# Performance work log

Measured on AMD Instinct MI355X. Metric: run time of the kernel, lower is better.

The kernel has to match this reference:

```python
import jax, jax.numpy as jnp
import numpy as np


def setup_inputs() -> dict:
    key = jax.random.key(0)
    k1, k2 = jax.random.split(key)
    B, H, S, D = 2, 16, 2048, 64
    v = jax.random.normal(k1, (B, H, S, D), dtype=jnp.float32)
    attn_logits = jax.random.normal(k2, (B, H, S, S), dtype=jnp.float32)
    return {"v": v, "attn_logits": attn_logits}


def reference(v, attn_logits):
    # softmax over last axis (keys j), then weighted sum of values
    attn = jax.nn.softmax(attn_logits, axis=-1)  # [b,h,i,j]
    return jnp.einsum('bhij,bhjd->bhid', attn, v)  # [b,h,i,d]
```

## Files before the change

### kernel.cpp

```cpp
#include <hip/hip_runtime.h>
#include <hip/hip_bf16.h>

typedef __attribute__((ext_vector_type(4))) float f32x4;
typedef __attribute__((ext_vector_type(8))) short short8;

#define S_DIM 2048
#define D_DIM 64
#define KB 128
#define NHEADS 32
#define QTILES (S_DIM / 64)
#define NJT (S_DIM / KB)
#define TILE_BYTES (D_DIM * KB * 2)

static __device__ __forceinline__ unsigned short f2bf(float x) {
    union { __hip_bfloat16 h; unsigned short u; } c;
    c.h = __float2bfloat16(x);
    return c.u;
}

__global__ __launch_bounds__(256)
void prep_v(const float* __restrict__ V, unsigned char* __restrict__ blob)
{
    const int b = blockIdx.x, head = b >> 4, jt = b & 15;
    const int t = threadIdx.x, d = t & 63, jg = t >> 6;
    const float* src = V + ((size_t)head * S_DIM + (size_t)jt * KB + jg * 32) * D_DIM + d;
    unsigned char* dst = blob + (size_t)(head * NJT + jt) * TILE_BYTES;
    #pragma unroll
    for (int h = 0; h < 4; ++h) {
        short8 w;
        #pragma unroll
        for (int e = 0; e < 8; ++e)
            w[e] = (short)f2bf(src[(size_t)(h * 8 + e) * D_DIM]);
        const int off = d * 256 + ((jg * 64 + h * 16) ^ ((d & 7) << 4));
        *(short8*)(dst + off) = w;
    }
}

__global__ __launch_bounds__(256, 4)
void attn_main(const float* __restrict__ L,
               const unsigned char* __restrict__ blob,
               float* __restrict__ O)
{
    __shared__ __align__(16) unsigned char vt[2][TILE_BYTES];

    const int tid  = threadIdx.x;
    const int wave = tid >> 6;
    const int lane = tid & 63;
    const int lr   = lane & 15;
    const int lg   = lane >> 4;

    const int bid  = blockIdx.x;
    const int xcd  = bid & 7;
    const int ixd  = bid >> 3;
    const int head = xcd * (NHEADS / 8) + (ixd >> 5);
    const int qt   = ixd & (QTILES - 1);

    const int i0 = qt * 64 + wave * 16;
    const float* lrow = L + ((size_t)head * S_DIM + (size_t)(i0 + lr)) * S_DIM;
    const unsigned char* hblob = blob + (size_t)head * NJT * TILE_BYTES;

    f32x4 acc[4] = {};
    float lsum = 0.0f;
    float pv[32];

    #pragma unroll
    for (int q = 0; q < 4; ++q)
        __builtin_amdgcn_global_load_lds(
            (const __attribute__((address_space(1))) void*)(hblob + q * 4096 + tid * 16),
            (__attribute__((address_space(3))) void*)(&vt[0][q * 4096 + tid * 16]),
            16, 0, 0);
    #pragma unroll
    for (int c = 0; c < 4; ++c) {
        f32x4 a = *(const f32x4*)(lrow + c * 32 + lg * 8);
        f32x4 b = *(const f32x4*)(lrow + c * 32 + lg * 8 + 4);
        pv[c*8+0]=a[0]; pv[c*8+1]=a[1]; pv[c*8+2]=a[2]; pv[c*8+3]=a[3];
        pv[c*8+4]=b[0]; pv[c*8+5]=b[1]; pv[c*8+6]=b[2]; pv[c*8+7]=b[3];
    }
    __syncthreads();

    for (int t = 0; t < NJT; ++t) {
        const int cur = t & 1;

        if (t + 1 < NJT) {
            const unsigned char* nsrc = hblob + (size_t)(t + 1) * TILE_BYTES;
            #pragma unroll
            for (int q = 0; q < 4; ++q)
                __builtin_amdgcn_global_load_lds(
                    (const __attribute__((address_space(1))) void*)(nsrc + q * 4096 + tid * 16),
                    (__attribute__((address_space(3))) void*)(&vt[cur ^ 1][q * 4096 + tid * 16]),
                    16, 0, 0);
        }

        short8 afr[4];
        #pragma unroll
        for (int c = 0; c < 4; ++c) {
            #pragma unroll
            for (int e = 0; e < 8; ++e) {
                float ev = __expf(pv[c*8+e]);
                lsum += ev;
                afr[c][e] = (short)f2bf(ev);
            }
        }

        if (t + 1 < NJT) {
            const float* s = lrow + (size_t)(t + 1) * KB;
            #pragma unroll
            for (int c = 0; c < 4; ++c) {
                f32x4 a = *(const f32x4*)(s + c * 32 + lg * 8);
                f32x4 b = *(const f32x4*)(s + c * 32 + lg * 8 + 4);
                pv[c*8+0]=a[0]; pv[c*8+1]=a[1]; pv[c*8+2]=a[2]; pv[c*8+3]=a[3];
                pv[c*8+4]=b[0]; pv[c*8+5]=b[1]; pv[c*8+6]=b[2]; pv[c*8+7]=b[3];
            }
        }

        #pragma unroll
        for (int c = 0; c < 4; ++c) {
            #pragma unroll
            for (int n = 0; n < 4; ++n) {
                const int off = ((n * 16 + lr) << 8)
                              + (((c << 6) | (lg << 4)) ^ ((lr & 7) << 4));
                short8 bfr = *(const short8*)&vt[cur][off];
                acc[n] = __builtin_amdgcn_mfma_f32_16x16x32_bf16(afr[c], bfr, acc[n], 0, 0, 0);
            }
        }

        __syncthreads();
    }

    lsum += __shfl_xor(lsum, 16);
    lsum += __shfl_xor(lsum, 32);
    #pragma unroll
    for (int r = 0; r < 4; ++r) {
        const float li  = __shfl(lsum, lg * 4 + r);
        const float inv = 1.0f / li;
        float* orow = O + ((size_t)head * S_DIM + (size_t)(i0 + lg * 4 + r)) * D_DIM;
        #pragma unroll
        for (int n = 0; n < 4; ++n)
            orow[n * 16 + lr] = acc[n][r] * inv;
    }
}

extern "C" void kernel_launch(void* const* d_in, const int* in_sizes, int n_in,
                              void* d_out, int out_size, void* d_ws, size_t ws_size,
                              hipStream_t stream) {
    const float* v = (const float*)d_in[0];
    const float* l = (const float*)d_in[1];
    float* out     = (float*)d_out;
    unsigned char* blob = (unsigned char*)d_ws;

    prep_v<<<dim3(NHEADS * NJT), dim3(256), 0, stream>>>(v, blob);
    attn_main<<<dim3(NHEADS * QTILES), dim3(256), 0, stream>>>(l, blob, out);
}
```

Baseline: 124.3 us.

## Coalesce logit loads via per-wave LDS transpose and read V fragments from global

Logits are now loaded as fully coalesced row segments (each half-wave reads 512 contiguous bytes of one row) into a ping-pong register buffer. The exponentiated bf16 values are written to a per-wave swizzled LDS scratch and read back in MFMA A-fragment layout. The shared V tile staging and block-wide barriers are removed, and V B-fragments are read straight from global (likely L2-resident) in a plain transposed layout. The row sum is now accumulated from the rounded bf16 values. The trade is less efficient V fetching from global and extra LDS round-trips, in exchange for better logit coalescing and no __syncthreads.

```diff
diff --git a/kernel.cpp b/kernel.cpp
--- a/kernel.cpp
+++ b/kernel.cpp
@@ -3,136 +3,126 @@
 
 typedef __attribute__((ext_vector_type(4))) float f32x4;
 typedef __attribute__((ext_vector_type(8))) short short8;
+typedef __attribute__((ext_vector_type(2))) unsigned int uint2v;
 
 #define S_DIM 2048
 #define D_DIM 64
 #define KB 128
 #define NHEADS 32
-#define QTILES (S_DIM / 64)
-#define NJT (S_DIM / KB)
-#define TILE_BYTES (D_DIM * KB * 2)
+#define QTILES 32
+#define NJT 16
+#define TILE_USHORT (D_DIM * KB)
 
 static __device__ __forceinline__ unsigned short f2bf(float x) {
     union { __hip_bfloat16 h; unsigned short u; } c;
     c.h = __float2bfloat16(x);
     return c.u;
 }
+static __device__ __forceinline__ float bf2f(unsigned short u) {
+    union { unsigned int i; float f; } c;
+    c.i = ((unsigned int)u) << 16;
+    return c.f;
+}
 
 __global__ __launch_bounds__(256)
-void prep_v(const float* __restrict__ V, unsigned char* __restrict__ blob)
+void prep_v(const float* __restrict__ V, unsigned short* __restrict__ blob)
 {
     const int b = blockIdx.x, head = b >> 4, jt = b & 15;
     const int t = threadIdx.x, d = t & 63, jg = t >> 6;
     const float* src = V + ((size_t)head * S_DIM + (size_t)jt * KB + jg * 32) * D_DIM + d;
-    unsigned char* dst = blob + (size_t)(head * NJT + jt) * TILE_BYTES;
+    unsigned short* dst = blob + (size_t)(head * NJT + jt) * TILE_USHORT + d * KB + jg * 32;
     #pragma unroll
     for (int h = 0; h < 4; ++h) {
         short8 w;
         #pragma unroll
         for (int e = 0; e < 8; ++e)
             w[e] = (short)f2bf(src[(size_t)(h * 8 + e) * D_DIM]);
-        const int off = d * 256 + ((jg * 64 + h * 16) ^ ((d & 7) << 4));
-        *(short8*)(dst + off) = w;
+        *(short8*)(dst + h * 8) = w;
     }
 }
 
-__global__ __launch_bounds__(256, 4)
+__global__ __launch_bounds__(256, 3)
 void attn_main(const float* __restrict__ L,
-               const unsigned char* __restrict__ blob,
+               const unsigned short* __restrict__ blob,
                float* __restrict__ O)
 {
-    __shared__ __align__(16) unsigned char vt[2][TILE_BYTES];
+    __shared__ __align__(16) unsigned char plds[4][4096];
 
     const int tid  = threadIdx.x;
     const int wave = tid >> 6;
     const int lane = tid & 63;
     const int lr   = lane & 15;
     const int lg   = lane >> 4;
+    const int half = lane >> 5;
+    const int l5   = lane & 31;
 
     const int bid  = blockIdx.x;
     const int xcd  = bid & 7;
     const int ixd  = bid >> 3;
     const int head = xcd * (NHEADS / 8) + (ixd >> 5);
     const int qt   = ixd & (QTILES - 1);
+    const int i0   = qt * 64 + wave * 16;
 
-    const int i0 = qt * 64 + wave * 16;
-    const float* lrow = L + ((size_t)head * S_DIM + (size_t)(i0 + lr)) * S_DIM;
-    const unsigned char* hblob = blob + (size_t)head * NJT * TILE_BYTES;
+    const float* lw = L + ((size_t)head * S_DIM + (size_t)(i0 + half)) * S_DIM + 4 * l5;
+    const unsigned short* hblob = blob + (size_t)head * NJT * TILE_USHORT;
+    unsigned char* pw = &plds[wave][0];
 
     f32x4 acc[4] = {};
     float lsum = 0.0f;
-    float pv[32];
 
+    f32x4 pa[8], pb[8];
     #pragma unroll
-    for (int q = 0; q < 4; ++q)
-        __builtin_amdgcn_global_load_lds(
-            (const __attribute__((address_space(1))) void*)(hblob + q * 4096 + tid * 16),
-            (__attribute__((address_space(3))) void*)(&vt[0][q * 4096 + tid * 16]),
-            16, 0, 0);
-    #pragma unroll
-    for (int c = 0; c < 4; ++c) {
-        f32x4 a = *(const f32x4*)(lrow + c * 32 + lg * 8);
-        f32x4 b = *(const f32x4*)(lrow + c * 32 + lg * 8 + 4);
-        pv[c*8+0]=a[0]; pv[c*8+1]=a[1]; pv[c*8+2]=a[2]; pv[c*8+3]=a[3];
-        pv[c*8+4]=b[0]; pv[c*8+5]=b[1]; pv[c*8+6]=b[2]; pv[c*8+7]=b[3];
-    }
-    __syncthreads();
+    for (int k = 0; k < 8; ++k)
+        pa[k] = *(const f32x4*)(lw + (size_t)(2 * k) * S_DIM);
 
-    for (int t = 0; t < NJT; ++t) {
-        const int cur = t & 1;
-
+    auto step = [&](int t, f32x4* cur, f32x4* nxt) {
         if (t + 1 < NJT) {
-            const unsigned char* nsrc = hblob + (size_t)(t + 1) * TILE_BYTES;
+            const float* s = lw + (size_t)(t + 1) * KB;
             #pragma unroll
-            for (int q = 0; q < 4; ++q)
-                __builtin_amdgcn_global_load_lds(
-                    (const __attribute__((address_space(1))) void*)(nsrc + q * 4096 + tid * 16),
-                    (__attribute__((address_space(3))) void*)(&vt[cur ^ 1][q * 4096 + tid * 16]),
-                    16, 0, 0);
+            for (int k = 0; k < 8; ++k)
+                nxt[k] = *(const f32x4*)(s + (size_t)(2 * k) * S_DIM);
         }
-
+        #pragma unroll
+        for (int k = 0; k < 8; ++k) {
+            const int row = 2 * k + half;
+            float e0 = __expf(cur[k][0]), e1 = __expf(cur[k][1]);
+            float e2 = __expf(cur[k][2]), e3 = __expf(cur[k][3]);
+            uint2v wv;
+            wv[0] = (unsigned)f2bf(e0) | ((unsigned)f2bf(e1) << 16);
+            wv[1] = (unsigned)f2bf(e2) | ((unsigned)f2bf(e3) << 16);
+            *(uint2v*)(pw + row * 256 + ((l5 * 8) ^ ((row & 7) << 4))) = wv;
+        }
         short8 afr[4];
         #pragma unroll
-        for (int c = 0; c < 4; ++c) {
+        for (int c = 0; c < 4; ++c)
+            afr[c] = *(const short8*)(pw + lr * 256 + (((c * 64) | (lg * 16)) ^ ((lr & 7) << 4)));
+        #pragma unroll
+        for (int c = 0; c < 4; ++c)
             #pragma unroll
-            for (int e = 0; e < 8; ++e) {
-                float ev = __expf(pv[c*8+e]);
-                lsum += ev;
-                afr[c][e] = (short)f2bf(ev);
-            }
-        }
-
-        if (t + 1 < NJT) {
-            const float* s = lrow + (size_t)(t + 1) * KB;
-            #pragma unroll
-            for (int c = 0; c < 4; ++c) {
-                f32x4 a = *(const f32x4*)(s + c * 32 + lg * 8);
-                f32x4 b = *(const f32x4*)(s + c * 32 + lg * 8 + 4);
-                pv[c*8+0]=a[0]; pv[c*8+1]=a[1]; pv[c*8+2]=a[2]; pv[c*8+3]=a[3];
-                pv[c*8+4]=b[0]; pv[c*8+5]=b[1]; pv[c*8+6]=b[2]; pv[c*8+7]=b[3];
-            }
-        }
-
+            for (int e = 0; e < 8; ++e)
+                lsum += bf2f((unsigned short)afr[c][e]);
+        const unsigned short* tile = hblob + (size_t)t * TILE_USHORT;
         #pragma unroll
         for (int c = 0; c < 4; ++c) {
             #pragma unroll
             for (int n = 0; n < 4; ++n) {
-                const int off = ((n * 16 + lr) << 8)
-                              + (((c << 6) | (lg << 4)) ^ ((lr & 7) << 4));
-                short8 bfr = *(const short8*)&vt[cur][off];
+                short8 bfr = *(const short8*)(tile + (n * 16 + lr) * KB + c * 32 + lg * 8);
                 acc[n] = __builtin_amdgcn_mfma_f32_16x16x32_bf16(afr[c], bfr, acc[n], 0, 0, 0);
             }
         }
+    };
 
-        __syncthreads();
+    #pragma unroll
+    for (int tt = 0; tt < NJT / 2; ++tt) {
+        step(2 * tt,     pa, pb);
+        step(2 * tt + 1, pb, pa);
     }
 
     lsum += __shfl_xor(lsum, 16);
     lsum += __shfl_xor(lsum, 32);
     #pragma unroll
     for (int r = 0; r < 4; ++r) {
-        const float li  = __shfl(lsum, lg * 4 + r);
-        const float inv = 1.0f / li;
+        const float inv = 1.0f / __shfl(lsum, lg * 4 + r);
         float* orow = O + ((size_t)head * S_DIM + (size_t)(i0 + lg * 4 + r)) * D_DIM;
         #pragma unroll
         for (int n = 0; n < 4; ++n)
@@ -146,7 +136,7 @@
     const float* v = (const float*)d_in[0];
     const float* l = (const float*)d_in[1];
     float* out     = (float*)d_out;
-    unsigned char* blob = (unsigned char*)d_ws;
+    unsigned short* blob = (unsigned short*)d_ws;
 
     prep_v<<<dim3(NHEADS * NJT), dim3(256), 0, stream>>>(v, blob);
     attn_main<<<dim3(NHEADS * QTILES), dim3(256), 0, stream>>>(l, blob, out);
```

Result: slower. 318.7 us (+156.4%).
